# Kernel optimization log

Measured on AMD Instinct MI355X. Metric: run time of the kernel, lower is better.

The kernel has to match this reference:

```python
import jax, jax.numpy as jnp
import numpy as np

NQ = 8            # data qubits: ceil(log2(256))
NLAYERS = 6       # StronglyEntanglingLayers depth
BATCH = 4096
IN_DIM = 2560
ENC_DIM = 256

def leaky(x):
    return jnp.where(x >= 0, x, 0.2 * x)

def rot_mat(phi, theta, omega):
    # PennyLane Rot(phi,theta,omega) = RZ(omega) @ RY(theta) @ RZ(phi)
    c = jnp.cos(theta / 2); s = jnp.sin(theta / 2)
    m00 = jnp.exp(-0.5j * (phi + omega)) * c
    m01 = -jnp.exp(0.5j * (phi - omega)) * s
    m10 = jnp.exp(-0.5j * (phi - omega)) * s
    m11 = jnp.exp(0.5j * (phi + omega)) * c
    return jnp.stack([jnp.stack([m00, m01]), jnp.stack([m10, m11])])

def apply_1q(psi, U, w):
    psi = jnp.tensordot(U, psi, axes=((1,), (w,)))
    return jnp.moveaxis(psi, 0, w)

def apply_cnot(psi, c, t):
    s = jnp.moveaxis(psi, (c, t), (0, 1))
    s = jnp.stack([s[0], s[1, ::-1]], axis=0)
    return jnp.moveaxis(s, (0, 1), (c, t))

def circuit(amps, params):
    # amps: (256,) complex64 normalized amplitudes; params: (L, NQ, 3)
    psi = amps.reshape((2,) * NQ)
    L = params.shape[0]
    for l in range(L):
        for q in range(NQ):
            psi = apply_1q(psi, rot_mat(params[l, q, 0], params[l, q, 1], params[l, q, 2]), q)
        r = l % (NQ - 1) + 1  # PennyLane default imprimitive ranges
        for q in range(NQ):
            psi = apply_cnot(psi, q, (q + r) % NQ)
    probs = jnp.real(psi * jnp.conj(psi))
    z, xm, ym = [], [], []
    yfac_base = jnp.array([-1j, 1j], dtype=psi.dtype)
    for q in range(NQ):
        axes = tuple(i for i in range(NQ) if i != q)
        p = jnp.sum(probs, axis=axes)
        z.append(p[0] - p[1])
        flipped = jnp.flip(psi, axis=q)
        xm.append(jnp.real(jnp.sum(jnp.conj(psi) * flipped)))
        yfac = yfac_base.reshape([2 if i == q else 1 for i in range(NQ)])
        ym.append(jnp.real(jnp.sum(jnp.conj(psi) * (flipped * yfac))))
    return jnp.stack(z + xm + ym)  # (24,) order: Z..., X..., Y...

def forward(x, ew1, eb1, ew2, eb2, ew3, eb3, dec_params,
            dw1, db1, dw2, db2, dw3, db3, dw4, db4, dw5, db5):
    h = leaky(x @ ew1 + eb1)
    h = leaky(h @ ew2 + eb2)
    enc = jnp.tanh(h @ ew3 + eb3)                      # (B, 256)
    nrm = jnp.linalg.norm(enc, axis=1, keepdims=True)
    amps = jax.lax.stop_gradient(enc / jnp.maximum(nrm, 1e-12)).astype(jnp.complex64)
    meas = jax.vmap(lambda a: circuit(a, dec_params))(amps)  # (B, 24)
    h = leaky(meas @ dw1 + db1)
    h = leaky(h @ dw2 + db2)
    h = leaky(h @ dw3 + db3)
    h = leaky(h @ dw4 + db4)
    return jnp.tanh(h @ dw5 + db5)                     # (B, 2560)

def _lin(key, fin, fout):
    k1, k2 = jax.random.split(key)
    lim = 1.0 / np.sqrt(fin)
    w = jax.random.uniform(k1, (fin, fout), jnp.float32, -lim, lim)
    b = jax.random.uniform(k2, (fout,), jnp.float32, -lim, lim)
    return w, b

def setup_inputs() -> dict:
    key = jax.random.key(0)
    ks = jax.random.split(key, 10)
    x = jax.random.normal(ks[0], (BATCH, IN_DIM), jnp.float32)
    ew1, eb1 = _lin(ks[1], IN_DIM, 1024)
    ew2, eb2 = _lin(ks[2], 1024, 512)
    ew3, eb3 = _lin(ks[3], 512, ENC_DIM)
    dec_params = jax.random.uniform(ks[4], (NLAYERS, NQ, 3), jnp.float32, 0.0, 2 * np.pi)
    dw1, db1 = _lin(ks[5], 3 * NQ, 128)
    dw2, db2 = _lin(ks[6], 128, 256)
    dw3, db3 = _lin(ks[7], 256, 512)
    dw4, db4 = _lin(ks[8], 512, 1024)
    dw5, db5 = _lin(ks[9], 1024, IN_DIM)
    return {"x": x, "ew1": ew1, "eb1": eb1, "ew2": ew2, "eb2": eb2, "ew3": ew3, "eb3": eb3,
            "dec_params": dec_params, "dw1": dw1, "db1": db1, "dw2": dw2, "db2": db2,
            "dw3": dw3, "db3": db3, "dw4": dw4, "db4": db4, "dw5": dw5, "db5": db5}

def reference(x, ew1, eb1, ew2, eb2, ew3, eb3, dec_params,
              dw1, db1, dw2, db2, dw3, db3, dw4, db4, dw5, db5):
    return forward(x, ew1, eb1, ew2, eb2, ew3, eb3, dec_params,
                   dw1, db1, dw2, db2, dw3, db3, dw4, db4, dw5, db5)
```

## Files before the change

### kernel.cpp

```cpp
#include <hip/hip_runtime.h>
#include <hip/hip_bf16.h>


using bf16 = __hip_bfloat16;
typedef __attribute__((ext_vector_type(8))) short short8;
typedef __attribute__((ext_vector_type(4))) short short4v;
typedef __attribute__((ext_vector_type(4))) float f32x4;

__device__ inline void stf(float* p, size_t i, float v) { p[i] = v; }
__device__ inline void stf(bf16* p, size_t i, float v) { p[i] = __float2bfloat16(v); }

__device__ inline short f2bs(float x) {
  bf16 h = __float2bfloat16(x);
  return *reinterpret_cast<short*>(&h);
}
__device__ inline short8 ld8b(const float* p) {
  const float4 a = ((const float4*)p)[0];
  const float4 b = ((const float4*)p)[1];
  short8 r;
  r[0] = f2bs(a.x); r[1] = f2bs(a.y); r[2] = f2bs(a.z); r[3] = f2bs(a.w);
  r[4] = f2bs(b.x); r[5] = f2bs(b.y); r[6] = f2bs(b.z); r[7] = f2bs(b.w);
  return r;
}
__device__ inline short4v ld4b(const float* p) {
  const float4 a = *(const float4*)p;
  short4v r;
  r[0] = f2bs(a.x); r[1] = f2bs(a.y); r[2] = f2bs(a.z); r[3] = f2bs(a.w);
  return r;
}

__device__ inline void async_load16(const bf16* g, short* l) {
  __builtin_amdgcn_global_load_lds(
      (const __attribute__((address_space(1))) unsigned int*)g,
      (__attribute__((address_space(3))) unsigned int*)l, 16, 0, 0);
}

__global__ __launch_bounds__(256) void cvt_f32_bf16(const float* __restrict__ in,
                                                    bf16* __restrict__ out, long n) {
  long i = ((long)blockIdx.x * 256 + threadIdx.x) * 8;
  if (i >= n) return;
  short8 v = ld8b(in + i);
  *(short8*)((short*)out + i) = v;
}

__global__ __launch_bounds__(256) void prep_all(
    const float* w0, const float* w1, const float* w2, const float* w3,
    const float* w4, const float* w5, const float* w6, const float* w7,
    const float* b0, const float* b1, const float* b2, const float* b3,
    const float* b4, const float* b5, const float* b6, const float* b7,
    const float* dp,
    bf16* __restrict__ wt, float* __restrict__ biasf, float* __restrict__ gw) {
  const int bid = blockIdx.x;
  const int tid = threadIdx.x;
  const int Ks[8]  = {2560, 1024, 512, 24, 128, 256, 512, 1024};
  const int Ns[8]  = {1024, 512, 256, 128, 256, 512, 1024, 2560};
  const int cum[8] = {2560, 3072, 3200, 3204, 3236, 3364, 3876, 6436};
  const long wto[8] = {0, 2621440, 3145728, 3276800, 3280896, 3313664, 3444736, 3969024};
  const float* Wp[8] = {w0, w1, w2, w3, w4, w5, w6, w7};
  const float* Bp[8] = {b0, b1, b2, b3, b4, b5, b6, b7};
  const int boff[8] = {0, 1024, 1536, 1792, 1920, 2176, 2688, 3712};

  if (bid < 6436) {
    int t = 0;
    while (bid >= cum[t]) t++;
    int base = t ? cum[t - 1] : 0;
    int local = bid - base;
    int K = Ks[t], N = Ns[t];
    int tk = (K + 31) >> 5;
    int kt = local % tk, nt = local / tk;
    int Kp = tk << 5;
    __shared__ short tile[32][33];
    int r = tid >> 3, c4 = (tid & 7) << 2;
    int gk = kt * 32 + r, gn = nt * 32 + c4;
    short4v v;
    if (gk < K) v = ld4b(Wp[t] + (size_t)gk * N + gn);
    else { v[0] = 0; v[1] = 0; v[2] = 0; v[3] = 0; }
    tile[r][c4] = v[0]; tile[r][c4 + 1] = v[1]; tile[r][c4 + 2] = v[2]; tile[r][c4 + 3] = v[3];
    __syncthreads();
    int n = tid >> 3, k4 = (tid & 7) << 2;
    short4v o;
    o[0] = tile[k4][n]; o[1] = tile[k4 + 1][n]; o[2] = tile[k4 + 2][n]; o[3] = tile[k4 + 3][n];
    *(short4v*)&wt[wto[t] + (size_t)(nt * 32 + n) * Kp + kt * 32 + k4] = o;
  } else if (bid < 6444) {
    int b = bid - 6436;
    int nb = Ns[b];
    for (int t2 = tid; t2 < nb; t2 += 256)
      biasf[boff[b] + t2] = Bp[b][t2];
  } else {
    int g = tid;
    if (g < 48) {
      float phi = dp[g * 3 + 0], theta = dp[g * 3 + 1], omega = dp[g * 3 + 2];
      float c = cosf(0.5f * theta), s = sinf(0.5f * theta);
      float a = 0.5f * (phi + omega), d = 0.5f * (phi - omega);
      float ca = cosf(a), sa = sinf(a), cd = cosf(d), sd = sinf(d);
      float* o = gw + g * 8;
      o[0] =  ca * c; o[1] = -sa * c;
      o[2] = -cd * s; o[3] = -sd * s;
      o[4] =  cd * s; o[5] = -sd * s;
      o[6] =  ca * c; o[7] =  sa * c;
    }
  }
}

template <int BM, int BN, int WR, int WC, int ACT, typename TC>
__global__ __launch_bounds__(256) void gemm_async(const bf16* __restrict__ A,
                                                  const bf16* __restrict__ Bt,
                                                  const float* __restrict__ bias,
                                                  TC* __restrict__ C,
                                                  int M, int N, int K) {
  constexpr int WMT = BM / WR;
  constexpr int WNT = BN / WC;
  constexpr int FI = WMT / 16;
  constexpr int FJ = WNT / 16;
  __shared__ __align__(16) short As[BM * 32];
  __shared__ __align__(16) short Bs[BN * 32];
  const int tid = threadIdx.x;
  const int lane = tid & 63;
  const int wid = tid >> 6;
  const int wm = wid / WC, wn = wid % WC;
  const int bm = blockIdx.y * BM;
  const int bn = blockIdx.x * BN;

  const int st_row = wid * 16 + (lane >> 2);
  const int st_col = (lane & 3) * 8;

  const int frag_m = lane & 15;
  const int frag_k = (lane >> 4) * 8;

  f32x4 acc[FI][FJ] = {};

  for (int k0 = 0; k0 < K; k0 += 32) {
#pragma unroll
    for (int c = 0; c < BM / 64; ++c) {
      const bf16* g = A + (size_t)(bm + c * 64 + st_row) * K + k0 + st_col;
      async_load16(g, &As[(c * 64 + wid * 16) * 32]);
    }
#pragma unroll
    for (int c = 0; c < BN / 64; ++c) {
      const bf16* g = Bt + (size_t)(bn + c * 64 + st_row) * K + k0 + st_col;
      async_load16(g, &Bs[(c * 64 + wid * 16) * 32]);
    }
    __syncthreads();
    short8 af[FI], bfr[FJ];
#pragma unroll
    for (int i = 0; i < FI; ++i)
      af[i] = *(const short8*)&As[(wm * WMT + i * 16 + frag_m) * 32 + frag_k];
#pragma unroll
    for (int j = 0; j < FJ; ++j)
      bfr[j] = *(const short8*)&Bs[(wn * WNT + j * 16 + frag_m) * 32 + frag_k];
#pragma unroll
    for (int i = 0; i < FI; ++i)
#pragma unroll
      for (int j = 0; j < FJ; ++j)
        acc[i][j] = __builtin_amdgcn_mfma_f32_16x16x32_bf16(af[i], bfr[j], acc[i][j], 0, 0, 0);
    __syncthreads();
  }

  const int col_lane = lane & 15;
  const int row_quad = (lane >> 4) << 2;
#pragma unroll
  for (int i = 0; i < FI; ++i) {
#pragma unroll
    for (int j = 0; j < FJ; ++j) {
      int n = bn + wn * WNT + j * 16 + col_lane;
      float bj = bias[n];
#pragma unroll
      for (int r = 0; r < 4; ++r) {
        int m = bm + wm * WMT + i * 16 + row_quad + r;
        float v = acc[i][j][r] + bj;
        if (ACT == 0) v = (v >= 0.f) ? v : 0.2f * v;
        else v = tanhf(v);
        stf(C, (size_t)m * N + n, v);
      }
    }
  }
}

__global__ __launch_bounds__(256) void gemm_cvt(const float* __restrict__ A,
                                                const float* __restrict__ W,
                                                const float* __restrict__ bias,
                                                bf16* __restrict__ C,
                                                int M, int N, int K) {
  __shared__ __align__(16) short As[128 * 40];
  __shared__ __align__(16) short Bs[128 * 40];
  const int tid = threadIdx.x;
  const int lane = tid & 63;
  const int wave = tid >> 6;
  const int wm = wave >> 1, wn = wave & 1;
  const int bm = blockIdx.y * 128;
  const int bn = blockIdx.x * 128;
  const int a_row0 = tid >> 2;
  const int a_kcol = (tid & 3) << 3;
  const int b_ncol = (tid & 31) << 2;
  const int b_krow = (tid >> 5) << 2;
  const int frag_m = lane & 15;
  const int frag_k = (lane >> 4) << 3;

  f32x4 acc[4][4] = {};

  for (int k0 = 0; k0 < K; k0 += 32) {
#pragma unroll
    for (int c = 0; c < 2; ++c) {
      const int row = c * 64 + a_row0;
      short8 v = ld8b(A + (size_t)(bm + row) * K + k0 + a_kcol);
      *(short8*)&As[row * 40 + a_kcol] = v;
    }
    short4v bv[4];
#pragma unroll
    for (int kk = 0; kk < 4; ++kk)
      bv[kk] = ld4b(W + (size_t)(k0 + b_krow + kk) * N + bn + b_ncol);
#pragma unroll
    for (int nn = 0; nn < 4; ++nn) {
      short4v w;
      w[0] = bv[0][nn]; w[1] = bv[1][nn]; w[2] = bv[2][nn]; w[3] = bv[3][nn];
      *(short4v*)&Bs[(b_ncol + nn) * 40 + b_krow] = w;
    }
    __syncthreads();
    short8 af[4], bfr[4];
#pragma unroll
    for (int i = 0; i < 4; ++i)
      af[i] = *(const short8*)&As[(wm * 64 + i * 16 + frag_m) * 40 + frag_k];
#pragma unroll
    for (int j = 0; j < 4; ++j)
      bfr[j] = *(const short8*)&Bs[(wn * 64 + j * 16 + frag_m) * 40 + frag_k];
#pragma unroll
    for (int i = 0; i < 4; ++i)
#pragma unroll
      for (int j = 0; j < 4; ++j)
        acc[i][j] = __builtin_amdgcn_mfma_f32_16x16x32_bf16(af[i], bfr[j], acc[i][j], 0, 0, 0);
    __syncthreads();
  }

  const int col_lane = lane & 15;
  const int row_quad = (lane >> 4) << 2;
#pragma unroll
  for (int i = 0; i < 4; ++i)
#pragma unroll
    for (int j = 0; j < 4; ++j) {
      int n = bn + wn * 64 + j * 16 + col_lane;
      float bj = bias[n];
#pragma unroll
      for (int r = 0; r < 4; ++r) {
        int m = bm + wm * 64 + i * 16 + row_quad + r;
        float v = acc[i][j][r] + bj;
        v = (v >= 0.f) ? v : 0.2f * v;
        stf(C, (size_t)m * N + n, v);
      }
    }
}

__global__ __launch_bounds__(256) void circuit_wave(const float* __restrict__ enc,
                                                    const float* __restrict__ gw,
                                                    bf16* __restrict__ meas) {
  __shared__ float gsh[384];
  const int tid = threadIdx.x;
  for (int t = tid; t < 384; t += 256) gsh[t] = gw[t];
  __syncthreads();
  const int lane = tid & 63;
  const int b = blockIdx.x * 4 + (tid >> 6);

  float4 e = *(const float4*)(enc + (size_t)b * 256 + lane * 4);
  float re[4] = {e.x, e.y, e.z, e.w};
  float im[4] = {0.f, 0.f, 0.f, 0.f};
  float ss = e.x * e.x + e.y * e.y + e.z * e.z + e.w * e.w;
#pragma unroll
  for (int o = 32; o; o >>= 1) ss += __shfl_xor(ss, o, 64);
  float inv = 1.0f / fmaxf(sqrtf(ss), 1e-12f);
#pragma unroll
  for (int j = 0; j < 4; ++j) re[j] *= inv;

  for (int l = 0; l < 6; ++l) {
    for (int q = 0; q < 8; ++q) {
      const float* g = &gsh[(l * 8 + q) * 8];
      const int s = 1 << (7 - q);
      if (s >= 4) {
        const int lm = s >> 2;
        const bool hi = (lane & lm) != 0;
        const float g0r = hi ? g[4] : g[0], g0i = hi ? g[5] : g[1];
        const float g1r = hi ? g[6] : g[2], g1i = hi ? g[7] : g[3];
#pragma unroll
        for (int j = 0; j < 4; ++j) {
          float orr = __shfl_xor(re[j], lm, 64);
          float oii = __shfl_xor(im[j], lm, 64);
          float p0r = hi ? orr : re[j], p0i = hi ? oii : im[j];
          float p1r = hi ? re[j] : orr, p1i = hi ? im[j] : oii;
          re[j] = g0r * p0r - g0i * p0i + g1r * p1r - g1i * p1i;
          im[j] = g0r * p0i + g0i * p0r + g1r * p1i + g1i * p1r;
        }
      } else {
#pragma unroll
        for (int j0 = 0; j0 < 4; ++j0) {
          if ((j0 & s) == 0) {
            int j1 = j0 | s;
            float p0r = re[j0], p0i = im[j0], p1r = re[j1], p1i = im[j1];
            re[j0] = g[0] * p0r - g[1] * p0i + g[2] * p1r - g[3] * p1i;
            im[j0] = g[0] * p0i + g[1] * p0r + g[2] * p1i + g[3] * p1r;
            re[j1] = g[4] * p0r - g[5] * p0i + g[6] * p1r - g[7] * p1i;
            im[j1] = g[4] * p0i + g[5] * p0r + g[6] * p1i + g[7] * p1r;
          }
        }
      }
    }
    const int r = l % 7 + 1;
    for (int q = 0; q < 8; ++q) {
      const int sc = 1 << (7 - q);
      const int st = 1 << (7 - ((q + r) & 7));
      if (st >= 4) {
        const int lm = st >> 2;
        if (sc >= 4) {
          const bool ctl = (lane & (sc >> 2)) != 0;
#pragma unroll
          for (int j = 0; j < 4; ++j) {
            float orr = __shfl_xor(re[j], lm, 64);
            float oii = __shfl_xor(im[j], lm, 64);
            re[j] = ctl ? orr : re[j];
            im[j] = ctl ? oii : im[j];
          }
        } else {
#pragma unroll
          for (int j = 0; j < 4; ++j) {
            if (j & sc) {
              re[j] = __shfl_xor(re[j], lm, 64);
              im[j] = __shfl_xor(im[j], lm, 64);
            }
          }
        }
      } else {
        if (sc >= 4) {
          const bool ctl = (lane & (sc >> 2)) != 0;
#pragma unroll
          for (int j0 = 0; j0 < 4; ++j0) {
            if ((j0 & st) == 0) {
              int j1 = j0 | st;
              float t0r = re[j0], t0i = im[j0];
              float t1r = re[j1], t1i = im[j1];
              re[j0] = ctl ? t1r : t0r; im[j0] = ctl ? t1i : t0i;
              re[j1] = ctl ? t0r : t1r; im[j1] = ctl ? t0i : t1i;
            }
          }
        } else {
#pragma unroll
          for (int j0 = 0; j0 < 4; ++j0) {
            if ((j0 & sc) && (j0 & st) == 0) {
              int j1 = j0 | st;
              float tr = re[j0], ti = im[j0];
              re[j0] = re[j1]; im[j0] = im[j1];
              re[j1] = tr; im[j1] = ti;
            }
          }
        }
      }
    }
  }

  for (int q = 0; q < 8; ++q) {
    const int s = 1 << (7 - q);
    float z = 0.f, x = 0.f, y = 0.f;
#pragma unroll
    for (int j = 0; j < 4; ++j) {
      float fr, fi;
      if (s >= 4) {
        fr = __shfl_xor(re[j], s >> 2, 64);
        fi = __shfl_xor(im[j], s >> 2, 64);
      } else {
        fr = re[j ^ s]; fi = im[j ^ s];
      }
      float prob = re[j] * re[j] + im[j] * im[j];
      int i = lane * 4 + j;
      float sg = (i & s) ? -1.f : 1.f;
      z += sg * prob;
      x += re[j] * fr + im[j] * fi;
      y += sg * (re[j] * fi - im[j] * fr);
    }
#pragma unroll
    for (int o = 32; o; o >>= 1) {
      z += __shfl_xor(z, o, 64);
      x += __shfl_xor(x, o, 64);
      y += __shfl_xor(y, o, 64);
    }
    if (lane == 0) {
      meas[(size_t)b * 32 + q]      = __float2bfloat16(z);
      meas[(size_t)b * 32 + 8 + q]  = __float2bfloat16(x);
      meas[(size_t)b * 32 + 16 + q] = __float2bfloat16(y);
    }
  }
  if (lane >= 24 && lane < 32)
    meas[(size_t)b * 32 + lane] = __float2bfloat16(0.f);
}

extern "C" void kernel_launch(void* const* d_in, const int* in_sizes, int n_in,
                              void* d_out, int out_size, void* d_ws, size_t ws_size,
                              hipStream_t stream) {
  (void)in_sizes; (void)n_in; (void)out_size;
  char* wsb = (char*)d_ws;
  float* gw    = (float*)(wsb + 256);
  float* biasf = (float*)(wsb + 4096);
  bf16*  meas  = (bf16*)(wsb + 32768);
  float* encf  = (float*)(wsb + 294912);
  bf16*  P     = (bf16*)(wsb + 4489216);
  bf16*  Q     = (bf16*)(wsb + 12877824);
  bf16*  WT    = (bf16*)(wsb + 17072128);
  bf16*  Xb    = (bf16*)(wsb + 30253056);
  const bool have_xb = ws_size >= 51224576;

  bf16* ew1t = WT + 0;
  bf16* ew2t = WT + 2621440;
  bf16* ew3t = WT + 3145728;
  bf16* dw1t = WT + 3276800;
  bf16* dw2t = WT + 3280896;
  bf16* dw3t = WT + 3313664;
  bf16* dw4t = WT + 3444736;
  bf16* dw5t = WT + 3969024;
  float* beb1 = biasf + 0;
  float* beb2 = biasf + 1024;
  float* beb3 = biasf + 1536;
  float* bdb1 = biasf + 1792;
  float* bdb2 = biasf + 1920;
  float* bdb3 = biasf + 2176;
  float* bdb4 = biasf + 2688;
  float* bdb5 = biasf + 3712;

  prep_all<<<6445, 256, 0, stream>>>(
      (const float*)d_in[1], (const float*)d_in[3], (const float*)d_in[5],
      (const float*)d_in[8], (const float*)d_in[10], (const float*)d_in[12],
      (const float*)d_in[14], (const float*)d_in[16],
      (const float*)d_in[2], (const float*)d_in[4], (const float*)d_in[6],
      (const float*)d_in[9], (const float*)d_in[11], (const float*)d_in[13],
      (const float*)d_in[15], (const float*)d_in[17],
      (const float*)d_in[7], WT, biasf, gw);

  if (have_xb) {
    cvt_f32_bf16<<<5120, 256, 0, stream>>>((const float*)d_in[0], Xb, 10485760L);
    gemm_async<128, 64, 4, 1, 0, bf16><<<dim3(16, 32), 256, 0, stream>>>(
        Xb, ew1t, beb1, P, 4096, 1024, 2560);
  } else {
    gemm_cvt<<<dim3(8, 32), 256, 0, stream>>>(
        (const float*)d_in[0], (const float*)d_in[1], beb1, P, 4096, 1024, 2560);
  }

  gemm_async<64, 64, 2, 2, 0, bf16><<<dim3(8, 64), 256, 0, stream>>>(
      P, ew2t, beb2, Q, 4096, 512, 1024);
  gemm_async<64, 64, 2, 2, 1, float><<<dim3(4, 64), 256, 0, stream>>>(
      Q, ew3t, beb3, encf, 4096, 256, 512);

  circuit_wave<<<1024, 256, 0, stream>>>(encf, gw, meas);

  gemm_async<64, 64, 2, 2, 0, bf16><<<dim3(2, 64), 256, 0, stream>>>(
      meas, dw1t, bdb1, Q, 4096, 128, 32);
  gemm_async<64, 64, 2, 2, 0, bf16><<<dim3(4, 64), 256, 0, stream>>>(
      Q, dw2t, bdb2, P, 4096, 256, 128);
  gemm_async<64, 64, 2, 2, 0, bf16><<<dim3(8, 64), 256, 0, stream>>>(
      P, dw3t, bdb3, Q, 4096, 512, 256);
  gemm_async<128, 64, 4, 1, 0, bf16><<<dim3(16, 32), 256, 0, stream>>>(
      Q, dw4t, bdb4, P, 4096, 1024, 512);
  gemm_async<128, 128, 2, 2, 1, float><<<dim3(20, 32), 256, 0, stream>>>(
      P, dw5t, bdb5, (float*)d_out, 4096, 2560, 1024);
}
```

Baseline: 322.4 us.

## Widen GEMM K-tile to 64 with XOR-swizzled LDS and fold input cast into prep

The GEMM template gains a BK parameter, and most layers now stage 64-wide K slices per barrier pair. This halves the number of syncthreads iterations and feeds two MFMAs per fragment load. LDS rows are XOR-swizzled by row to avoid bank conflicts at the wider stride. The separate f32-to-bf16 input conversion kernel is merged into prep_all as extra blocks, which saves a launch. The cost is doubled LDS use per block, which may lower occupancy.

```diff
diff --git a/kernel.cpp b/kernel.cpp
--- a/kernel.cpp
+++ b/kernel.cpp
@@ -35,21 +35,14 @@
       (__attribute__((address_space(3))) unsigned int*)l, 16, 0, 0);
 }
 
-__global__ __launch_bounds__(256) void cvt_f32_bf16(const float* __restrict__ in,
-                                                    bf16* __restrict__ out, long n) {
-  long i = ((long)blockIdx.x * 256 + threadIdx.x) * 8;
-  if (i >= n) return;
-  short8 v = ld8b(in + i);
-  *(short8*)((short*)out + i) = v;
-}
-
 __global__ __launch_bounds__(256) void prep_all(
     const float* w0, const float* w1, const float* w2, const float* w3,
     const float* w4, const float* w5, const float* w6, const float* w7,
     const float* b0, const float* b1, const float* b2, const float* b3,
     const float* b4, const float* b5, const float* b6, const float* b7,
-    const float* dp,
-    bf16* __restrict__ wt, float* __restrict__ biasf, float* __restrict__ gw) {
+    const float* dp, const float* xf,
+    bf16* __restrict__ wt, float* __restrict__ biasf, float* __restrict__ gw,
+    bf16* __restrict__ xb, int do_x) {
   const int bid = blockIdx.x;
   const int tid = threadIdx.x;
   const int Ks[8]  = {2560, 1024, 512, 24, 128, 256, 512, 1024};
@@ -86,7 +79,7 @@
     int nb = Ns[b];
     for (int t2 = tid; t2 < nb; t2 += 256)
       biasf[boff[b] + t2] = Bp[b][t2];
-  } else {
+  } else if (bid == 6444) {
     int g = tid;
     if (g < 48) {
       float phi = dp[g * 3 + 0], theta = dp[g * 3 + 1], omega = dp[g * 3 + 2];
@@ -99,21 +92,32 @@
       o[4] =  cd * s; o[5] = -sd * s;
       o[6] =  ca * c; o[7] =  sa * c;
     }
-  }
-}
-
-template <int BM, int BN, int WR, int WC, int ACT, typename TC>
+  } else if (do_x) {
+    long i = ((long)(bid - 6445) * 256 + tid) * 8;
+    if (i < 10485760L) {
+      short8 v = ld8b(xf + i);
+      *(short8*)((short*)xb + i) = v;
+    }
+  }
+}
+
+template <int BM, int BN, int BK, int WR, int WC, int ACT, typename TC>
 __global__ __launch_bounds__(256) void gemm_async(const bf16* __restrict__ A,
                                                   const bf16* __restrict__ Bt,
                                                   const float* __restrict__ bias,
                                                   TC* __restrict__ C,
                                                   int M, int N, int K) {
+  constexpr int CPR = BK / 8;
+  constexpr int MASK = CPR - 1;
+  constexpr int RPW = 64 / CPR;
+  constexpr int RPP = 4 * RPW;
   constexpr int WMT = BM / WR;
   constexpr int WNT = BN / WC;
   constexpr int FI = WMT / 16;
   constexpr int FJ = WNT / 16;
-  __shared__ __align__(16) short As[BM * 32];
-  __shared__ __align__(16) short Bs[BN * 32];
+  constexpr int KK = BK / 32;
+  __shared__ __align__(16) short As[BM * BK];
+  __shared__ __align__(16) short Bs[BN * BK];
   const int tid = threadIdx.x;
   const int lane = tid & 63;
   const int wid = tid >> 6;
@@ -121,43 +125,57 @@
   const int bm = blockIdx.y * BM;
   const int bn = blockIdx.x * BN;
 
-  const int st_row = wid * 16 + (lane >> 2);
-  const int st_col = (lane & 3) * 8;
+  const int st_r = lane / CPR;
+  const int st_cs = (lane & MASK) ^ (st_r & MASK);
 
   const int frag_m = lane & 15;
-  const int frag_k = (lane >> 4) * 8;
+  const int q = lane >> 4;
 
   f32x4 acc[FI][FJ] = {};
 
-  for (int k0 = 0; k0 < K; k0 += 32) {
-#pragma unroll
-    for (int c = 0; c < BM / 64; ++c) {
-      const bf16* g = A + (size_t)(bm + c * 64 + st_row) * K + k0 + st_col;
-      async_load16(g, &As[(c * 64 + wid * 16) * 32]);
-    }
-#pragma unroll
-    for (int c = 0; c < BN / 64; ++c) {
-      const bf16* g = Bt + (size_t)(bn + c * 64 + st_row) * K + k0 + st_col;
-      async_load16(g, &Bs[(c * 64 + wid * 16) * 32]);
+  for (int k0 = 0; k0 < K; k0 += BK) {
+#pragma unroll
+    for (int p = 0; p < BM / RPP; ++p) {
+      const bf16* g = A + (size_t)(bm + p * RPP + wid * RPW + st_r) * K + k0 + st_cs * 8;
+      async_load16(g, &As[(p * RPP + wid * RPW) * BK]);
+    }
+#pragma unroll
+    for (int p = 0; p < BN / RPP; ++p) {
+      const bf16* g = Bt + (size_t)(bn + p * RPP + wid * RPW + st_r) * K + k0 + st_cs * 8;
+      async_load16(g, &Bs[(p * RPP + wid * RPW) * BK]);
     }
     __syncthreads();
-    short8 af[FI], bfr[FJ];
-#pragma unroll
-    for (int i = 0; i < FI; ++i)
-      af[i] = *(const short8*)&As[(wm * WMT + i * 16 + frag_m) * 32 + frag_k];
-#pragma unroll
-    for (int j = 0; j < FJ; ++j)
-      bfr[j] = *(const short8*)&Bs[(wn * WNT + j * 16 + frag_m) * 32 + frag_k];
-#pragma unroll
-    for (int i = 0; i < FI; ++i)
-#pragma unroll
-      for (int j = 0; j < FJ; ++j)
-        acc[i][j] = __builtin_amdgcn_mfma_f32_16x16x32_bf16(af[i], bfr[j], acc[i][j], 0, 0, 0);
+    short8 af[FI][KK], bfr[FJ][KK];
+#pragma unroll
+    for (int i = 0; i < FI; ++i) {
+      const int m = wm * WMT + i * 16 + frag_m;
+#pragma unroll
+      for (int kk = 0; kk < KK; ++kk) {
+        const int slot = (kk * 4 + q) ^ (m & MASK);
+        af[i][kk] = *(const short8*)&As[m * BK + slot * 8];
+      }
+    }
+#pragma unroll
+    for (int j = 0; j < FJ; ++j) {
+      const int n = wn * WNT + j * 16 + frag_m;
+#pragma unroll
+      for (int kk = 0; kk < KK; ++kk) {
+        const int slot = (kk * 4 + q) ^ (n & MASK);
+        bfr[j][kk] = *(const short8*)&Bs[n * BK + slot * 8];
+      }
+    }
+#pragma unroll
+    for (int kk = 0; kk < KK; ++kk)
+#pragma unroll
+      for (int i = 0; i < FI; ++i)
+#pragma unroll
+        for (int j = 0; j < FJ; ++j)
+          acc[i][j] = __builtin_amdgcn_mfma_f32_16x16x32_bf16(af[i][kk], bfr[j][kk], acc[i][j], 0, 0, 0);
     __syncthreads();
   }
 
   const int col_lane = lane & 15;
-  const int row_quad = (lane >> 4) << 2;
+  const int row_quad = q << 2;
 #pragma unroll
   for (int i = 0; i < FI; ++i) {
 #pragma unroll
@@ -270,9 +288,9 @@
   for (int j = 0; j < 4; ++j) re[j] *= inv;
 
   for (int l = 0; l < 6; ++l) {
-    for (int q = 0; q < 8; ++q) {
-      const float* g = &gsh[(l * 8 + q) * 8];
-      const int s = 1 << (7 - q);
+    for (int qq = 0; qq < 8; ++qq) {
+      const float* g = &gsh[(l * 8 + qq) * 8];
+      const int s = 1 << (7 - qq);
       if (s >= 4) {
         const int lm = s >> 2;
         const bool hi = (lane & lm) != 0;
@@ -302,9 +320,9 @@
       }
     }
     const int r = l % 7 + 1;
-    for (int q = 0; q < 8; ++q) {
-      const int sc = 1 << (7 - q);
-      const int st = 1 << (7 - ((q + r) & 7));
+    for (int qq = 0; qq < 8; ++qq) {
+      const int sc = 1 << (7 - qq);
+      const int st = 1 << (7 - ((qq + r) & 7));
       if (st >= 4) {
         const int lm = st >> 2;
         if (sc >= 4) {
@@ -353,8 +371,8 @@
     }
   }
 
-  for (int q = 0; q < 8; ++q) {
-    const int s = 1 << (7 - q);
+  for (int qq = 0; qq < 8; ++qq) {
+    const int s = 1 << (7 - qq);
     float z = 0.f, x = 0.f, y = 0.f;
 #pragma unroll
     for (int j = 0; j < 4; ++j) {
@@ -379,9 +397,9 @@
       y += __shfl_xor(y, o, 64);
     }
     if (lane == 0) {
-      meas[(size_t)b * 32 + q]      = __float2bfloat16(z);
-      meas[(size_t)b * 32 + 8 + q]  = __float2bfloat16(x);
-      meas[(size_t)b * 32 + 16 + q] = __float2bfloat16(y);
+      meas[(size_t)b * 32 + qq]      = __float2bfloat16(z);
+      meas[(size_t)b * 32 + 8 + qq]  = __float2bfloat16(x);
+      meas[(size_t)b * 32 + 16 + qq] = __float2bfloat16(y);
     }
   }
   if (lane >= 24 && lane < 32)
@@ -420,39 +438,39 @@
   float* bdb4 = biasf + 2688;
   float* bdb5 = biasf + 3712;
 
-  prep_all<<<6445, 256, 0, stream>>>(
+  prep_all<<<11565, 256, 0, stream>>>(
       (const float*)d_in[1], (const float*)d_in[3], (const float*)d_in[5],
       (const float*)d_in[8], (const float*)d_in[10], (const float*)d_in[12],
       (const float*)d_in[14], (const float*)d_in[16],
       (const float*)d_in[2], (const float*)d_in[4], (const float*)d_in[6],
       (const float*)d_in[9], (const float*)d_in[11], (const float*)d_in[13],
       (const float*)d_in[15], (const float*)d_in[17],
-      (const float*)d_in[7], WT, biasf, gw);
+      (const float*)d_in[7], (const float*)d_in[0],
+      WT, biasf, gw, Xb, have_xb ? 1 : 0);
 
   if (have_xb) {
-    cvt_f32_bf16<<<5120, 256, 0, stream>>>((const float*)d_in[0], Xb, 10485760L);
-    gemm_async<128, 64, 4, 1, 0, bf16><<<dim3(16, 32), 256, 0, stream>>>(
+    gemm_async<128, 64, 64, 4, 1, 0, bf16><<<dim3(16, 32), 256, 0, stream>>>(
         Xb, ew1t, beb1, P, 4096, 1024, 2560);
   } else {
     gemm_cvt<<<dim3(8, 32), 256, 0, stream>>>(
         (const float*)d_in[0], (const float*)d_in[1], beb1, P, 4096, 1024, 2560);
   }
 
-  gemm_async<64, 64, 2, 2, 0, bf16><<<dim3(8, 64), 256, 0, stream>>>(
+  gemm_async<64, 64, 64, 2, 2, 0, bf16><<<dim3(8, 64), 256, 0, stream>>>(
       P, ew2t, beb2, Q, 4096, 512, 1024);
-  gemm_async<64, 64, 2, 2, 1, float><<<dim3(4, 64), 256, 0, stream>>>(
+  gemm_async<64, 64, 64, 2, 2, 1, float><<<dim3(4, 64), 256, 0, stream>>>(
       Q, ew3t, beb3, encf, 4096, 256, 512);
 
   circuit_wave<<<1024, 256, 0, stream>>>(encf, gw, meas);
 
-  gemm_async<64, 64, 2, 2, 0, bf16><<<dim3(2, 64), 256, 0, stream>>>(
+  gemm_async<64, 64, 32, 2, 2, 0, bf16><<<dim3(2, 64), 256, 0, stream>>>(
       meas, dw1t, bdb1, Q, 4096, 128, 32);
-  gemm_async<64, 64, 2, 2, 0, bf16><<<dim3(4, 64), 256, 0, stream>>>(
+  gemm_async<64, 64, 64, 2, 2, 0, bf16><<<dim3(4, 64), 256, 0, stream>>>(
       Q, dw2t, bdb2, P, 4096, 256, 128);
-  gemm_async<64, 64, 2, 2, 0, bf16><<<dim3(8, 64), 256, 0, stream>>>(
+  gemm_async<64, 64, 64, 2, 2, 0, bf16><<<dim3(8, 64), 256, 0, stream>>>(
       P, dw3t, bdb3, Q, 4096, 512, 256);
-  gemm_async<128, 64, 4, 1, 0, bf16><<<dim3(16, 32), 256, 0, stream>>>(
+  gemm_async<128, 64, 64, 4, 1, 0, bf16><<<dim3(16, 32), 256, 0, stream>>>(
       Q, dw4t, bdb4, P, 4096, 1024, 512);
-  gemm_async<128, 128, 2, 2, 1, float><<<dim3(20, 32), 256, 0, stream>>>(
+  gemm_async<128, 128, 64, 2, 2, 1, float><<<dim3(20, 32), 256, 0, stream>>>(
       P, dw5t, bdb5, (float*)d_out, 4096, 2560, 1024);
 }
```

New measurement: 309.8 us. 1.04x faster.
